# Optimization experiments

Hardware: AMD Instinct MI355X
Metric: run time of the kernel (lower is better)

Reference implementation:

```python
import jax, jax.numpy as jnp
import numpy as np
from jax import lax

EPS = 1e-5

def _conv(x, w, b):
    # sign-binarized conv: sign(x) conv sign(w) + float bias; 3x3, pad 1, NCHW
    y = lax.conv_general_dilated(jnp.sign(x), jnp.sign(w), (1, 1), ((1, 1), (1, 1)),
                                 dimension_numbers=("NCHW", "OIHW", "NCHW"))
    return y + b[None, :, None, None]

def _bn(x, g, beta, mean, var):
    # eval-mode batchnorm with running stats
    inv = g / jnp.sqrt(var + EPS)
    return x * inv[None, :, None, None] + (beta - mean * inv)[None, :, None, None]

def _pool2(x):
    return lax.reduce_window(x, -jnp.inf, lax.max, (1, 1, 2, 2), (1, 1, 2, 2), "VALID")

def setup_inputs() -> dict:
    key = jax.random.key(0)
    ks = jax.random.split(key, 16)
    B, num_classes = 4096, 2
    x = jax.random.normal(ks[0], (B, 1, 64, 64), dtype=jnp.float32)
    def conv_params(k, cout, cin):
        k1, k2 = jax.random.split(k)
        w = jax.random.normal(k1, (cout, cin, 3, 3), dtype=jnp.float32) * 0.1
        b = jax.random.normal(k2, (cout,), dtype=jnp.float32) * 0.01
        return w, b
    def bn_params(k, c):
        k1, k2, k3 = jax.random.split(k, 3)
        g = 1.0 + 0.1 * jax.random.normal(k1, (c,), dtype=jnp.float32)
        beta = 0.1 * jax.random.normal(k2, (c,), dtype=jnp.float32)
        mean = 0.1 * jax.random.normal(k3, (c,), dtype=jnp.float32)
        var = jnp.ones((c,), dtype=jnp.float32)
        return g, beta, mean, var
    w1, b1 = conv_params(ks[1], 8, 1)
    w2, b2 = conv_params(ks[2], 16, 8)
    w3, b3 = conv_params(ks[3], 32, 16)
    g1, be1, m1, v1 = bn_params(ks[4], 8)
    g2, be2, m2, v2 = bn_params(ks[5], 16)
    g3, be3, m3, v3 = bn_params(ks[6], 32)
    fc_w = jax.random.normal(ks[7], (num_classes, 32 * 8 * 8), dtype=jnp.float32) * 0.02
    fc_b = jnp.zeros((num_classes,), dtype=jnp.float32)
    return dict(x=x, w1=w1, b1=b1, g1=g1, be1=be1, m1=m1, v1=v1,
                w2=w2, b2=b2, g2=g2, be2=be2, m2=m2, v2=v2,
                w3=w3, b3=b3, g3=g3, be3=be3, m3=m3, v3=v3,
                fc_w=fc_w, fc_b=fc_b)

def reference(x, w1, b1, g1, be1, m1, v1,
              w2, b2, g2, be2, m2, v2,
              w3, b3, g3, be3, m3, v3, fc_w, fc_b):
    h = _pool2(jax.nn.relu(_bn(_conv(x, w1, b1), g1, be1, m1, v1)))   # [B,8,32,32]
    h = _pool2(jax.nn.relu(_bn(_conv(h, w2, b2), g2, be2, m2, v2)))   # [B,16,16,16]
    h = _pool2(jax.nn.relu(_bn(_conv(h, w3, b3), g3, be3, m3, v3)))   # [B,32,8,8]
    h = h.reshape(h.shape[0], -1)                                      # [B,2048]
    logits = h @ fc_w.T + fc_b
    return jax.nn.softmax(logits, axis=1)
```

## Files before the change

kernel.cpp:

```cpp
#include <hip/hip_runtime.h>
#include <stdint.h>

#define EPS 1e-5f
typedef unsigned long long u64;
typedef unsigned int u32;
typedef unsigned short u16;
typedef unsigned char u8;

struct Consts {
  u32 p2r[16][4];
  u64 q3m0[32];
  u64 q3m1[32];
  u32 q3m2[32];
  int lo2[16];
  u32 rng2[16];
  float inv3[32];
  float A3[32];
  float b3v[32];
  float fcb[2];
  u8  lut[9 * 512];
};
static_assert(sizeof(Consts) == 6024, "layout");

__global__ void prep_kernel(
    const float* __restrict__ w1, const float* __restrict__ b1,
    const float* __restrict__ g1, const float* __restrict__ be1,
    const float* __restrict__ m1, const float* __restrict__ v1,
    const float* __restrict__ w2, const float* __restrict__ b2,
    const float* __restrict__ g2, const float* __restrict__ be2,
    const float* __restrict__ m2, const float* __restrict__ v2,
    const float* __restrict__ w3, const float* __restrict__ b3,
    const float* __restrict__ g3, const float* __restrict__ be3,
    const float* __restrict__ m3, const float* __restrict__ v3,
    const float* __restrict__ fcb, Consts* __restrict__ out)
{
  int tid = threadIdx.x;

  if (blockIdx.x == 0) {
    if (tid < 16) {
      int c = tid;
      u32 rm[3] = {0u, 0u, 0u};
      for (int ci = 0; ci < 8; ++ci)
        for (int t = 0; t < 9; ++t) {
          float w = w2[(c * 8 + ci) * 9 + t];
          if (w > 0.f) rm[t / 3] |= 1u << ((t % 3) * 8 + ci);
        }
      out->p2r[c][0] = rm[0]; out->p2r[c][1] = rm[1];
      out->p2r[c][2] = rm[2]; out->p2r[c][3] = 0u;
      float inv = __fdiv_rn(g2[c], __fsqrt_rn(__fadd_rn(v2[c], EPS)));
      float A   = __fsub_rn(be2[c], __fmul_rn(m2[c], inv));
      int lo = 1000, hi = -1000;
      for (int s = -72; s <= 72; ++s) {
        float y  = __fadd_rn((float)s, b2[c]);
        float bn = __fadd_rn(__fmul_rn(y, inv), A);
        if (bn > 0.f) { if (s < lo) lo = s; if (s > hi) hi = s; }
      }
      out->lo2[c] = lo; out->rng2[c] = (u32)(hi - lo);
    }
    if (tid < 32) {
      int c = tid;
      u64 q0 = 0, q1 = 0; u32 q2 = 0;
      for (int ci = 0; ci < 16; ++ci)
        for (int t = 0; t < 9; ++t) {
          float w = w3[(c * 16 + ci) * 9 + t];
          if (w > 0.f) {
            if (t < 4)      q0 |= 1ull << (t * 16 + ci);
            else if (t < 8) q1 |= 1ull << ((t - 4) * 16 + ci);
            else            q2 |= 1u << ci;
          }
        }
      out->q3m0[c] = q0; out->q3m1[c] = q1; out->q3m2[c] = q2;
      float inv = __fdiv_rn(g3[c], __fsqrt_rn(__fadd_rn(v3[c], EPS)));
      out->inv3[c] = inv;
      out->A3[c]   = __fsub_rn(be3[c], __fmul_rn(m3[c], inv));
      out->b3v[c]  = b3[c];
    }
    if (tid < 2) out->fcb[tid] = fcb[tid];
    return;
  }

  __shared__ float inv1s[8], A1s[8];
  __shared__ int   sw1[8][9];
  if (tid < 8) {
    int c = tid;
    float inv = __fdiv_rn(g1[c], __fsqrt_rn(__fadd_rn(v1[c], EPS)));
    inv1s[c] = inv;
    A1s[c]   = __fsub_rn(be1[c], __fmul_rn(m1[c], inv));
    for (int t = 0; t < 9; ++t) sw1[c][t] = (w1[c * 9 + t] > 0.f) ? 1 : -1;
  }
  __syncthreads();
  int e = (blockIdx.x - 1) * 256 + tid;
  int type = e >> 9, pat = e & 511;
  int ty = type / 3, tx = type % 3;
  u8 byte = 0;
  for (int c = 0; c < 8; ++c) {
    int s = 0;
    for (int t = 0; t < 9; ++t) {
      int dr = t / 3, dc = t % 3;
      bool valid = !((ty == 0 && dr == 0) || (ty == 2 && dr == 2) ||
                     (tx == 0 && dc == 0) || (tx == 2 && dc == 2));
      if (!valid) continue;
      s += ((pat >> t) & 1) ? sw1[c][t] : -sw1[c][t];
    }
    float y  = __fadd_rn((float)s, b1[c]);
    float bn = __fadd_rn(__fmul_rn(y, inv1s[c]), A1s[c]);
    if (bn > 0.f) byte |= (u8)(1u << c);
  }
  out->lut[e] = byte;
}

__launch_bounds__(256, 4)
__global__ void main_kernel(const float* __restrict__ x, const float* __restrict__ fcw,
                            const Consts* __restrict__ cs, float* __restrict__ out, int B)
{
  __shared__ __align__(16) u8  slut[9 * 512];
  __shared__ __align__(16) u64 xb[2][64];
  __shared__ __align__(16) u8  s2p[2][34][36];
  __shared__ __align__(16) u16 s3p[2][18][18];
  __shared__ float red[2][2][2];

  const int tid = threadIdx.x;
  const int wv = tid >> 6, lane = tid & 63;
  const int im = wv >> 1, w = wv & 1;
  const int img = blockIdx.x * 2 + im;

  for (int i = tid; i < 1152; i += 256) ((u32*)slut)[i] = ((const u32*)cs->lut)[i];
  for (int i = tid; i < 612; i += 256) ((u32*)s2p)[i] = 0;
  for (int i = tid; i < 324; i += 256) ((u32*)s3p)[i] = 0;

  if (img < B) {
    const float* xp = x + (size_t)img * 4096 + (size_t)w * 2048;
    u64 my = 0;
    #pragma unroll 4
    for (int rr = 0; rr < 32; ++rr) {
      float v = xp[rr * 64 + lane];
      u64 m = __ballot(v > 0.f);
      if (lane == rr) my = m;
    }
    if (lane < 32) xb[im][w * 32 + lane] = my;
  }
  __syncthreads();

  {
    const int c = lane & 31, h = lane >> 5;
    const int j0 = 2 * c;
    const u32 tj0 = (c == 0) ? 0u : 1u;
    const u32 tj1 = (c == 31) ? 2u : 1u;
    #pragma unroll
    for (int p = 0; p < 8; ++p) {
      const int pr = w * 16 + h * 8 + p;
      const int i0 = 2 * pr;
      u64 r0 = (i0 > 0) ? xb[im][i0 - 1] : 0ull;
      u64 r1 = xb[im][i0];
      u64 r2 = xb[im][i0 + 1];
      u64 r3 = (i0 + 2 < 64) ? xb[im][i0 + 2] : 0ull;
      u32 acc = 0;
      #pragma unroll
      for (int a = 0; a < 2; ++a) {
        u64 ra = a ? r1 : r0, rb = a ? r2 : r1, rc = a ? r3 : r2;
        const int i = i0 + a;
        const u32 ti3 = ((i == 0) ? 0u : ((i == 63) ? 2u : 1u)) * 3u;
        u32 pat0;
        if (j0 == 0) {
          pat0 = (((u32)ra << 1) & 6u) | ((((u32)rb << 1) & 6u) << 3) |
                 ((((u32)rc << 1) & 6u) << 6);
        } else {
          pat0 = ((u32)(ra >> (j0 - 1)) & 7u) | (((u32)(rb >> (j0 - 1)) & 7u) << 3) |
                 (((u32)(rc >> (j0 - 1)) & 7u) << 6);
        }
        acc |= slut[((ti3 + tj0) << 9) | pat0];
        u32 pat1 = ((u32)(ra >> j0) & 7u) | (((u32)(rb >> j0) & 7u) << 3) |
                   (((u32)(rc >> j0) & 7u) << 6);
        acc |= slut[((ti3 + tj1) << 9) | pat1];
      }
      s2p[im][pr + 1][c + 1] = (u8)acc;
    }
  }
  __syncthreads();

  {
    const int idx = w * 64 + lane;
    const int pi = idx >> 3, pjp = idx & 7;
    const int bo = 4 * pjp;
    const u32* rp0 = (const u32*)&s2p[im][2 * pi + 0][bo];
    const u32* rp1 = (const u32*)&s2p[im][2 * pi + 1][bo];
    const u32* rp2 = (const u32*)&s2p[im][2 * pi + 2][bo];
    const u32* rp3 = (const u32*)&s2p[im][2 * pi + 3][bo];
    u32 rl[4], rh[4];
    rl[0] = rp0[0]; rh[0] = rp0[1];
    rl[1] = rp1[0]; rh[1] = rp1[1];
    rl[2] = rp2[0]; rh[2] = rp2[1];
    rl[3] = rp3[0]; rh[3] = rp3[1];

    u32 d0[8], d1[8], d2[8]; int pc[8]; u32 cw[8];
    #pragma unroll
    for (int k = 0; k < 8; ++k) {
      const int o = k >> 2, a = (k >> 1) & 1, bb = k & 1;
      const int sh = 8 * (2 * o + bb);
      d0[k] = __builtin_amdgcn_alignbit(rh[a],     rl[a],     sh) & 0xFFFFFFu;
      d1[k] = __builtin_amdgcn_alignbit(rh[a + 1], rl[a + 1], sh) & 0xFFFFFFu;
      d2[k] = __builtin_amdgcn_alignbit(rh[a + 2], rl[a + 2], sh) & 0xFFFFFFu;
      pc[k] = __popc(d0[k]) + __popc(d1[k]) + __popc(d2[k]);
      cw[k] = 0u;
    }

    #pragma unroll 1
    for (int ch = 15; ch >= 0; --ch) {
      const u32 m0 = cs->p2r[ch][0];
      const u32 m1 = cs->p2r[ch][1];
      const u32 m2 = cs->p2r[ch][2];
      const int nlo = -cs->lo2[ch];
      const u32 rng = cs->rng2[ch];
      #pragma unroll
      for (int k = 0; k < 8; ++k) {
        int ps = __popc(d0[k] & m0) + __popc(d1[k] & m1) + __popc(d2[k] & m2);
        u32 t = (u32)(2 * ps - pc[k] + nlo);
        cw[k] = cw[k] + cw[k] + ((t <= rng) ? 1u : 0u);
      }
    }
    s3p[im][pi + 1][2 * pjp + 1] = (u16)(cw[0] | cw[1] | cw[2] | cw[3]);
    s3p[im][pi + 1][2 * pjp + 2] = (u16)(cw[4] | cw[5] | cw[6] | cw[7]);
  }
  __syncthreads();

  float l0 = 0.f, l1 = 0.f;
  {
    const int pi = lane >> 3, pj = lane & 7;
    const u32* p0 = (const u32*)(&s3p[im][2 * pi + 0][2 * pj]);
    const u32* p1 = (const u32*)(&s3p[im][2 * pi + 1][2 * pj]);
    const u32* p2 = (const u32*)(&s3p[im][2 * pi + 2][2 * pj]);
    const u32* p3 = (const u32*)(&s3p[im][2 * pi + 3][2 * pj]);
    const u64 rr0 = (u64)p0[0] | ((u64)p0[1] << 32);
    const u64 rr1 = (u64)p1[0] | ((u64)p1[1] << 32);
    const u64 rr2 = (u64)p2[0] | ((u64)p2[1] << 32);
    const u64 rr3 = (u64)p3[0] | ((u64)p3[1] << 32);

    u64 q0a, q1a, q0b, q1b, q0c, q1c, q0d, q1d;
    u32 q2a, q2b, q2c, q2d;
    int pca, pcb, pcc, pcd;
    {
      u64 ta, tb, tc;
      ta = rr0;       tb = rr1;       tc = rr2;
      q0a = (ta & 0xFFFFFFFFFFFFull) | ((tb & 0xFFFFull) << 48);
      q1a = ((tb >> 16) & 0xFFFFFFFFull) | ((tc & 0xFFFFFFFFull) << 32);
      q2a = (u32)((tc >> 32) & 0xFFFFull);
      pca = __popcll(q0a) + __popcll(q1a) + __popc(q2a);
      ta = rr0 >> 16; tb = rr1 >> 16; tc = rr2 >> 16;
      q0b = (ta & 0xFFFFFFFFFFFFull) | ((tb & 0xFFFFull) << 48);
      q1b = ((tb >> 16) & 0xFFFFFFFFull) | ((tc & 0xFFFFFFFFull) << 32);
      q2b = (u32)((tc >> 32) & 0xFFFFull);
      pcb = __popcll(q0b) + __popcll(q1b) + __popc(q2b);
      ta = rr1;       tb = rr2;       tc = rr3;
      q0c = (ta & 0xFFFFFFFFFFFFull) | ((tb & 0xFFFFull) << 48);
      q1c = ((tb >> 16) & 0xFFFFFFFFull) | ((tc & 0xFFFFFFFFull) << 32);
      q2c = (u32)((tc >> 32) & 0xFFFFull);
      pcc = __popcll(q0c) + __popcll(q1c) + __popc(q2c);
      ta = rr1 >> 16; tb = rr2 >> 16; tc = rr3 >> 16;
      q0d = (ta & 0xFFFFFFFFFFFFull) | ((tb & 0xFFFFull) << 48);
      q1d = ((tb >> 16) & 0xFFFFFFFFull) | ((tc & 0xFFFFFFFFull) << 32);
      q2d = (u32)((tc >> 32) & 0xFFFFull);
      pcd = __popcll(q0d) + __popcll(q1d) + __popc(q2d);
    }

    #pragma unroll 2
    for (int cc = 0; cc < 16; ++cc) {
      const int c = 16 * w + cc;
      const u64 m0 = cs->q3m0[c], m1 = cs->q3m1[c];
      const u32 m2 = cs->q3m2[c];
      int t0 = 2 * (__popcll(q0a & m0) + __popcll(q1a & m1) + __popc(q2a & m2)) - pca;
      int t1 = 2 * (__popcll(q0b & m0) + __popcll(q1b & m1) + __popc(q2b & m2)) - pcb;
      int t2 = 2 * (__popcll(q0c & m0) + __popcll(q1c & m1) + __popc(q2c & m2)) - pcc;
      int t3 = 2 * (__popcll(q0d & m0) + __popcll(q1d & m1) + __popc(q2d & m2)) - pcd;
      int smax = max(max(t0, t1), max(t2, t3));
      int smin = min(min(t0, t1), min(t2, t3));
      float inv = cs->inv3[c];
      int sel = (inv > 0.f) ? smax : smin;
      float y   = __fadd_rn((float)sel, cs->b3v[c]);
      float bn  = __fadd_rn(__fmul_rn(y, inv), cs->A3[c]);
      float val = fmaxf(bn, 0.f);
      const int f = (c << 6) + lane;
      l0 = fmaf(val, fcw[f], l0);
      l1 = fmaf(val, fcw[2048 + f], l1);
    }
  }

  #pragma unroll
  for (int d = 32; d >= 1; d >>= 1) {
    l0 += __shfl_xor(l0, d, 64);
    l1 += __shfl_xor(l1, d, 64);
  }
  if (lane == 0) { red[im][w][0] = l0; red[im][w][1] = l1; }
  __syncthreads();
  if ((tid & 127) == 0 && img < B) {
    float a0 = red[im][0][0] + red[im][1][0] + cs->fcb[0];
    float a1 = red[im][0][1] + red[im][1][1] + cs->fcb[1];
    float mm = fmaxf(a0, a1);
    float e0 = expf(a0 - mm), e1 = expf(a1 - mm);
    float sden = e0 + e1;
    out[(size_t)img * 2]     = e0 / sden;
    out[(size_t)img * 2 + 1] = e1 / sden;
  }
}

extern "C" void kernel_launch(void* const* d_in, const int* in_sizes, int n_in,
                              void* d_out, int out_size, void* d_ws, size_t ws_size,
                              hipStream_t stream) {
  const float* x   = (const float*)d_in[0];
  const float* w1  = (const float*)d_in[1];
  const float* b1  = (const float*)d_in[2];
  const float* g1  = (const float*)d_in[3];
  const float* be1 = (const float*)d_in[4];
  const float* m1  = (const float*)d_in[5];
  const float* v1  = (const float*)d_in[6];
  const float* w2  = (const float*)d_in[7];
  const float* b2  = (const float*)d_in[8];
  const float* g2  = (const float*)d_in[9];
  const float* be2 = (const float*)d_in[10];
  const float* m2  = (const float*)d_in[11];
  const float* v2  = (const float*)d_in[12];
  const float* w3  = (const float*)d_in[13];
  const float* b3  = (const float*)d_in[14];
  const float* g3  = (const float*)d_in[15];
  const float* be3 = (const float*)d_in[16];
  const float* m3  = (const float*)d_in[17];
  const float* v3  = (const float*)d_in[18];
  const float* fcw = (const float*)d_in[19];
  const float* fcb = (const float*)d_in[20];

  int B = in_sizes[0] / 4096;
  Consts* cs = (Consts*)d_ws;

  prep_kernel<<<19, 256, 0, stream>>>(w1, b1, g1, be1, m1, v1,
                                      w2, b2, g2, be2, m2, v2,
                                      w3, b3, g3, be3, m3, v3, fcb, cs);
  int nblk = (B + 1) / 2;
  main_kernel<<<nblk, 256, 0, stream>>>(x, fcw, cs, (float*)d_out, B);
}
```

Before: 69.03 us.

## Replace block barriers with per-image wave-pair LDS flag sync; simplify conv1 pattern indexing

Swaps the four block-wide __syncthreads between stages for a pair_sync that uses an LDS atomic counter per image. Only the two waves working on the same image wait for each other, so the two images in a block no longer stall on one another. It also rewrites the conv1 pattern extraction into branch-free per-lane shift, mask and base constants. The spin-wait with s_sleep and the extra atomics add overhead and could be slower than hardware barriers. The extra initial __syncthreads also adds one barrier.

```diff
diff --git a/kernel.cpp b/kernel.cpp
--- a/kernel.cpp
+++ b/kernel.cpp
@@ -109,6 +109,13 @@
   out->lut[e] = byte;
 }
 
+__device__ __forceinline__ void pair_sync(u32* flag, int lane, u32 target) {
+  __threadfence_block();
+  if (lane == 0) atomicAdd(flag, 1u);
+  while (*(volatile u32*)flag < target) __builtin_amdgcn_s_sleep(2);
+  __threadfence_block();
+}
+
 __launch_bounds__(256, 4)
 __global__ void main_kernel(const float* __restrict__ x, const float* __restrict__ fcw,
                             const Consts* __restrict__ cs, float* __restrict__ out, int B)
@@ -118,6 +125,7 @@
   __shared__ __align__(16) u8  s2p[2][34][36];
   __shared__ __align__(16) u16 s3p[2][18][18];
   __shared__ float red[2][2][2];
+  __shared__ u32 bar[2];
 
   const int tid = threadIdx.x;
   const int wv = tid >> 6, lane = tid & 63;
@@ -127,6 +135,8 @@
   for (int i = tid; i < 1152; i += 256) ((u32*)slut)[i] = ((const u32*)cs->lut)[i];
   for (int i = tid; i < 612; i += 256) ((u32*)s2p)[i] = 0;
   for (int i = tid; i < 324; i += 256) ((u32*)s3p)[i] = 0;
+  if (tid < 2) bar[tid] = 0u;
+  __syncthreads();
 
   if (img < B) {
     const float* xp = x + (size_t)img * 4096 + (size_t)w * 2048;
@@ -139,13 +149,16 @@
     }
     if (lane < 32) xb[im][w * 32 + lane] = my;
   }
-  __syncthreads();
+  pair_sync(&bar[im], lane, 2u);
 
   {
     const int c = lane & 31, h = lane >> 5;
     const int j0 = 2 * c;
-    const u32 tj0 = (c == 0) ? 0u : 1u;
-    const u32 tj1 = (c == 31) ? 2u : 1u;
+    const u32 sa0  = (c == 0) ? 0u : (u32)(j0 - 1);
+    const u32 msk0 = (c == 0) ? 3u : 7u;
+    const u32 sft0 = (c == 0) ? 1u : 0u;
+    const u32 base0 = ((c == 0) ? 0u : 1u) << 9;
+    const u32 base1 = ((c == 31) ? 2u : 1u) << 9;
     #pragma unroll
     for (int p = 0; p < 8; ++p) {
       const int pr = w * 16 + h * 8 + p;
@@ -159,24 +172,20 @@
       for (int a = 0; a < 2; ++a) {
         u64 ra = a ? r1 : r0, rb = a ? r2 : r1, rc = a ? r3 : r2;
         const int i = i0 + a;
-        const u32 ti3 = ((i == 0) ? 0u : ((i == 63) ? 2u : 1u)) * 3u;
-        u32 pat0;
-        if (j0 == 0) {
-          pat0 = (((u32)ra << 1) & 6u) | ((((u32)rb << 1) & 6u) << 3) |
-                 ((((u32)rc << 1) & 6u) << 6);
-        } else {
-          pat0 = ((u32)(ra >> (j0 - 1)) & 7u) | (((u32)(rb >> (j0 - 1)) & 7u) << 3) |
-                 (((u32)(rc >> (j0 - 1)) & 7u) << 6);
-        }
-        acc |= slut[((ti3 + tj0) << 9) | pat0];
-        u32 pat1 = ((u32)(ra >> j0) & 7u) | (((u32)(rb >> j0) & 7u) << 3) |
-                   (((u32)(rc >> j0) & 7u) << 6);
-        acc |= slut[((ti3 + tj1) << 9) | pat1];
+        const u32 ti9 = ((i == 0) ? 0u : ((i == 63) ? 6u : 3u)) << 9;
+        u32 ea = ((u32)(ra >> sa0) & msk0) << sft0;
+        u32 eb = ((u32)(rb >> sa0) & msk0) << sft0;
+        u32 ec = ((u32)(rc >> sa0) & msk0) << sft0;
+        acc |= slut[ti9 + base0 + (ea | (eb << 3) | (ec << 6))];
+        u32 fa = (u32)(ra >> j0) & 7u;
+        u32 fb = (u32)(rb >> j0) & 7u;
+        u32 fc = (u32)(rc >> j0) & 7u;
+        acc |= slut[ti9 + base1 + (fa | (fb << 3) | (fc << 6))];
       }
       s2p[im][pr + 1][c + 1] = (u8)acc;
     }
   }
-  __syncthreads();
+  pair_sync(&bar[im], lane, 4u);
 
   {
     const int idx = w * 64 + lane;
@@ -221,7 +230,7 @@
     s3p[im][pi + 1][2 * pjp + 1] = (u16)(cw[0] | cw[1] | cw[2] | cw[3]);
     s3p[im][pi + 1][2 * pjp + 2] = (u16)(cw[4] | cw[5] | cw[6] | cw[7]);
   }
-  __syncthreads();
+  pair_sync(&bar[im], lane, 6u);
 
   float l0 = 0.f, l1 = 0.f;
   {
@@ -290,8 +299,8 @@
     l1 += __shfl_xor(l1, d, 64);
   }
   if (lane == 0) { red[im][w][0] = l0; red[im][w][1] = l1; }
-  __syncthreads();
-  if ((tid & 127) == 0 && img < B) {
+  pair_sync(&bar[im], lane, 8u);
+  if (w == 0 && lane == 0 && img < B) {
     float a0 = red[im][0][0] + red[im][1][0] + cs->fcb[0];
     float a1 = red[im][0][1] + red[im][1][1] + cs->fcb[1];
     float mm = fmaxf(a0, a1);
```

Result: faster. 67.55 us (-2.1%).
